# Performance work log

Measured on AMD Instinct MI355X. Metric: run time of the kernel, lower is better.

## Reference

```python
import jax, jax.numpy as jnp
import numpy as np

N, D, GN, UVW = 64, 32, 128, 64
EMB = H = 256
NONSP, SPA = 8, 2
ACT = NONSP + 4          # 12
GOA = 256 + ACT          # fc3 + action = 268
GLO = H + GOA            # 524
SW = 64


def _conv3(x, w, b):
    # 3x3, stride 1, pad 1, NCHW / OIHW (torch layout)
    y = jax.lax.conv_general_dilated(x, w, (1, 1), ((1, 1), (1, 1)),
                                     dimension_numbers=('NCHW', 'OIHW', 'NCHW'))
    return y + b[None, :, None, None]


def _up2(x):
    # bilinear x2, half-pixel centers (matches torch align_corners=False)
    n, c, h, w = x.shape
    return jax.image.resize(x, (n, c, 2 * h, 2 * w), 'bilinear')


def setup_inputs() -> dict:
    key = jax.random.key(0)
    ks = jax.random.split(key, 24)
    def rn(k, shape, s=0.05):
        return jax.random.normal(k, shape, jnp.float32) * s
    G = (jax.random.uniform(ks[0], (N, D, GN, GN)) < 0.1).astype(jnp.float32)
    avail = jax.random.randint(ks[2], (N, NONSP), 0, 2).astype(jnp.int32)
    avail = avail.at[:, 0].set(1)  # guarantee at least one available action
    return {
        'G': G,
        'X': rn(ks[1], (N, D, GN, UVW), 1.0),
        'avail_actions': avail,
        'LSTM_hidden': jnp.zeros((2, 1, N, H), jnp.float32),
        'prev_actions': rn(ks[3], (N, D, ACT), 1.0),
        'relevant_frames': jax.random.randint(ks[4], (N, D), 0, 2).astype(jnp.int32),
        'We': rn(ks[5], (UVW, EMB)), 'be': jnp.zeros((EMB,)),
        'W1': rn(ks[6], (EMB, 256)), 'b1': jnp.zeros((256,)),
        'W2': rn(ks[7], (256, 256)), 'b2': jnp.zeros((256,)),
        'W3': rn(ks[8], (256, 256)), 'b3': jnp.zeros((256,)),
        'Wle': rn(ks[9], (GOA, H)), 'ble': jnp.zeros((H,)),
        'Wih': rn(ks[10], (4 * H, H)), 'Whh': rn(ks[11], (4 * H, H)),
        'bih': jnp.zeros((4 * H,)), 'bhh': jnp.zeros((4 * H,)),
        'Wa': rn(ks[12], (GLO, NONSP)), 'ba': jnp.zeros((NONSP,)),
        'Wv': rn(ks[13], (GLO, 1)), 'bv': jnp.zeros((1,)),
        'Wt1': rn(ks[14], (GLO, 256, 4, 4)), 'bt1': jnp.zeros((256,)),
        'Wc2': rn(ks[15], (128, 256, 3, 3)), 'bc2': jnp.zeros((128,)),
        'Wc3': rn(ks[16], (64, 128, 3, 3)), 'bc3': jnp.zeros((64,)),
        'Wc4': rn(ks[17], (64, 64, 3, 3)), 'bc4': jnp.zeros((64,)),
        'Wc5': rn(ks[18], (64, 64, 3, 3)), 'bc5': jnp.zeros((64,)),
        'Wc6': rn(ks[19], (SPA, 64, 3, 3)), 'bc6': jnp.zeros((SPA,)),
    }


def reference(G, X, avail_actions, LSTM_hidden, prev_actions, relevant_frames,
              We, be, W1, b1, W2, b2, W3, b3, Wle, ble, Wih, Whh, bih, bhh,
              Wa, ba, Wv, bv, Wt1, bt1, Wc2, bc2, Wc3, bc3, Wc4, bc4,
              Wc5, bc5, Wc6, bc6):
    n = G.shape[0]
    eye = jnp.eye(GN, dtype=G.dtype)

    def step(carry, xs):
        h, c, _, _ = carry
        Gc, Xc, pa, rel = xs            # [n,GN,GN], [n,GN,UVW], [n,ACT], [n]
        A = Gc + eye
        dis = 1.0 / jnp.sqrt(jnp.maximum(A.sum(-1), 1.0))
        A_agg = A * dis[:, :, None] * dis[:, None, :]  # D^-1/2 A D^-1/2
        emb = jnp.tanh(Xc @ We + be)
        h1 = jnp.tanh(A_agg @ (emb @ W1 + b1))
        h2 = jnp.tanh(A_agg @ (h1 @ W2 + b2))
        h3 = jnp.tanh(A_agg @ (h2 @ W3 + b3))
        goa = jnp.concatenate([h3.max(axis=1), pa], axis=1)  # [n, GOA]
        xin = jnp.tanh(goa @ Wle + ble)
        gates = xin @ Wih.T + bih + h @ Whh.T + bhh
        i, f, g, o = jnp.split(gates, 4, axis=1)
        c_new = jax.nn.sigmoid(f) * c + jax.nn.sigmoid(i) * jnp.tanh(g)
        h_new = jax.nn.sigmoid(o) * jnp.tanh(c_new)
        keep = (rel != 0).astype(h_new.dtype)[:, None]  # reset hidden for irrelevant frames
        return (h_new * keep, c_new * keep, h_new, goa), None

    h0, c0 = LSTM_hidden[0, 0], LSTM_hidden[1, 0]
    goa0 = jnp.zeros((n, GOA), G.dtype)
    xs = (jnp.swapaxes(G, 0, 1), jnp.swapaxes(X, 0, 1),
          jnp.swapaxes(prev_actions, 0, 1), jnp.swapaxes(relevant_frames, 0, 1))
    (hf, cf, hout, goa), _ = jax.lax.scan(step, (h0, c0, h0, goa0), xs)

    glo = jnp.concatenate([hout, goa], axis=1)  # [n, 524]
    logits = glo @ Wa + ba
    logits = jnp.where(avail_actions == 0, -jnp.inf, logits)
    nonspatial_policy = jax.nn.softmax(logits, axis=1)
    value = glo @ Wv + bv

    # deconv on 1x1 input == einsum with torch [in,out,kh,kw] weight
    s1 = jax.nn.leaky_relu(jnp.einsum('nc,cfhw->nfhw', glo, Wt1) + bt1[None, :, None, None], 0.1)
    # note: original F.relu(x, 0.1) is plain relu (0.1 lands in `inplace`)
    s2 = jax.nn.relu(_up2(_conv3(s1, Wc2, bc2)))
    s3 = jax.nn.relu(_up2(_conv3(s2, Wc3, bc3)))
    s4 = jax.nn.relu(_up2(_conv3(s3, Wc4, bc4)))
    s5 = jax.nn.relu(_up2(_conv3(s4, Wc5, bc5)))
    sl = _conv3(s5, Wc6, bc6).reshape(n, SPA, -1)
    spatial_policy = jax.nn.softmax(sl, axis=2).reshape(n, SPA, SW, SW)

    LSTM_hidden_out = jnp.stack([hf, cf])[:, None]  # [2,1,n,H]
    return (spatial_policy, nonspatial_policy, value, LSTM_hidden_out)
```

## Files before the change

### kernel.cpp

```cpp
#include <hip/hip_runtime.h>
#include <math.h>

typedef unsigned short u16;
typedef unsigned int u32;

typedef __attribute__((ext_vector_type(8))) short bf16x8;
typedef __attribute__((ext_vector_type(4))) float f32x4;

__device__ __forceinline__ float b2f(u16 u) {
    union { u32 ui; float f; } v; v.ui = ((u32)u) << 16; return v.f;
}
__device__ __forceinline__ float b2f_lo(u32 u) {
    union { u32 ui; float f; } v; v.ui = u << 16; return v.f;
}
__device__ __forceinline__ float b2f_hi(u32 u) {
    union { u32 ui; float f; } v; v.ui = u & 0xffff0000u; return v.f;
}
__device__ __forceinline__ u16 f2b(float f) {
    union { float f; u32 ui; } v; v.f = f;
    u32 x = v.ui;
    u32 r = (x + 0x7fffu + ((x >> 16) & 1u)) >> 16;
    return (u16)r;
}
__device__ __forceinline__ float sigf(float x) { return 1.0f / (1.0f + expf(-x)); }
__device__ __forceinline__ float ftanh(float x) {
    float e = __expf(2.0f * x);
    return 1.0f - 2.0f / (e + 1.0f);
}

#define GNODES 128
#define EMBD   256
#define NB     64
#define TS     32
#define GOA    268
#define GLO    524

#define OUT_SPATIAL 0
#define OUT_NS      524288
#define OUT_V       524800
#define OUT_H       524864

#define WS_GOA   ((size_t)0)
#define WS_HBUF  ((size_t)2195456)
#define WS_CBUF  ((size_t)2260992)
#define WS_HOUT  ((size_t)2326528)
#define WS_GLO   ((size_t)2392064)
#define WS_WIHT  ((size_t)2526208)
#define WS_WHHT  ((size_t)3574784)
#define WS_BSUM  ((size_t)4623360)
#define WS_C2    ((size_t)4627456)
#define WS_C3    ((size_t)4889600)
#define WS_C4    ((size_t)5413888)
#define WS_C5    ((size_t)7511040)
#define WS_SL    ((size_t)15899648)
#define WS_WET   ((size_t)16948224)
#define WS_W1T   ((size_t)16980992)
#define WS_W2T   ((size_t)17112064)
#define WS_W3T   ((size_t)17243136)
#define WS_GX    ((size_t)17374208)
#define WS_S1F   ((size_t)25762816)

#define WS_WP4   WS_GOA
#define WS_WP5   (WS_GOA + (size_t)196608)
#define WS_WP3   (WS_GOA + (size_t)393216)
#define WS_WP2   WS_GX

#define SA_S 264
#define TT_S 136
#define XS_S 72

__global__ void wprep(const float* __restrict__ We, const float* __restrict__ W1,
                      const float* __restrict__ W2, const float* __restrict__ W3,
                      u16* __restrict__ WeT, u16* __restrict__ W1T,
                      u16* __restrict__ W2T, u16* __restrict__ W3T)
{
    int idx = blockIdx.x * 256 + threadIdx.x;
    if (idx < 16384) {
        int k = idx >> 8, nn = idx & 255;
        WeT[nn * 64 + k] = f2b(We[idx]);
    }
    {
        int k = idx >> 8, nn = idx & 255;
        W1T[nn * 256 + k] = f2b(W1[idx]);
        W2T[nn * 256 + k] = f2b(W2[idx]);
        W3T[nn * 256 + k] = f2b(W3[idx]);
    }
}

__global__ __launch_bounds__(1024, 4) void gcn_mfma(
    const float* __restrict__ G, const float* __restrict__ X, const float* __restrict__ pa,
    const u16* __restrict__ WeT, const float* __restrict__ be,
    const u16* __restrict__ W1T, const float* __restrict__ b1,
    const u16* __restrict__ W2T, const float* __restrict__ b2,
    const u16* __restrict__ W3T, const float* __restrict__ b3,
    float* __restrict__ goaAll)
{
    __shared__ u16 Sa[128 * SA_S];
    __shared__ u16 Tt[256 * TT_S];
    __shared__ float dis[GNODES];
    __shared__ float dred[1024];
    __shared__ float pm[256];

    const int item = blockIdx.x;
    const int tid  = threadIdx.x;
    const int wv   = tid >> 6;
    const int nt   = wv & 7;
    const int ch   = wv >> 3;
    const int lane = tid & 63;
    const int l16  = lane & 15;
    const int quad = lane >> 4;
    const float* Gp = G + (size_t)item * GNODES * GNODES;
    const float* Xp = X + (size_t)item * GNODES * 64;

    for (int idx = tid; idx < 128 * 64; idx += 1024) {
        int m = idx >> 6, k = idx & 63;
        Tt[m * XS_S + k] = f2b(Xp[idx]);
    }
    {
        int row = tid >> 3, part = tid & 7;
        const float4* gr = (const float4*)(Gp + (size_t)row * GNODES) + part * 4;
        float s = 0.f;
#pragma unroll
        for (int k = 0; k < 4; ++k) { float4 g = gr[k]; s += g.x + g.y + g.z + g.w; }
        dred[tid] = s;
    }
    __syncthreads();
    if (tid < GNODES) {
        float s = 0.f;
#pragma unroll
        for (int p = 0; p < 8; ++p) s += dred[tid * 8 + p];
        dis[tid] = 1.0f / sqrtf(s + 1.0f);
    }
    __syncthreads();

    bf16x8 bAgg[4];
    {
        const int i = nt * 16 + l16;
        const float di = dis[i];
        const float* gr = Gp + (size_t)i * GNODES;
#pragma unroll
        for (int t = 0; t < 4; ++t) {
            const int k0 = t * 32 + quad * 8;
            float4 ga = *(const float4*)(gr + k0);
            float4 gb = *(const float4*)(gr + k0 + 4);
            float vv[8] = {ga.x, ga.y, ga.z, ga.w, gb.x, gb.y, gb.z, gb.w};
            bf16x8 f;
#pragma unroll
            for (int j = 0; j < 8; ++j) {
                int k = k0 + j;
                float a = (vv[j] + (k == i ? 1.0f : 0.0f)) * di * dis[k];
                f[j] = (short)f2b(a);
            }
            bAgg[t] = f;
        }
    }

    {
        bf16x8 a0 = *(const bf16x8*)(Tt + (16 * nt + l16) * XS_S + quad * 8);
        bf16x8 a1 = *(const bf16x8*)(Tt + (16 * nt + l16) * XS_S + 32 + quad * 8);
        for (int cj = 0; cj < 8; ++cj) {
            const int ct = ch * 8 + cj;
            const int nf = ct * 16 + l16;
            bf16x8 wb0 = *(const bf16x8*)(WeT + nf * 64 + quad * 8);
            bf16x8 wb1 = *(const bf16x8*)(WeT + nf * 64 + 32 + quad * 8);
            float bb = be[nf];
            f32x4 acc = {bb, bb, bb, bb};
            acc = __builtin_amdgcn_mfma_f32_16x16x32_bf16(a0, wb0, acc, 0, 0, 0);
            acc = __builtin_amdgcn_mfma_f32_16x16x32_bf16(a1, wb1, acc, 0, 0, 0);
#pragma unroll
            for (int r = 0; r < 4; ++r) {
                int node = 16 * nt + quad * 4 + r;
                Sa[node * SA_S + nf] = f2b(ftanh(acc[r]));
            }
        }
    }
    __syncthreads();

    const u16* WTs[3]  = {W1T, W2T, W3T};
    const float* bss[3] = {b1, b2, b3};

    for (int l = 0; l < 3; ++l) {
        const u16* WT = WTs[l];
        const float* bias = bss[l];

        const int nf = wv * 16 + l16;
        const float bb = bias[nf];
        bf16x8 bfr[8];
#pragma unroll
        for (int t = 0; t < 8; ++t)
            bfr[t] = *(const bf16x8*)(WT + (size_t)nf * 256 + t * 32 + quad * 8);

        for (int rt = 0; rt < 8; ++rt) {
            bf16x8 afr[8];
#pragma unroll
            for (int t = 0; t < 8; ++t)
                afr[t] = *(const bf16x8*)(Sa + (16 * rt + l16) * SA_S + t * 32 + quad * 8);
            f32x4 acc = {bb, bb, bb, bb};
#pragma unroll
            for (int t = 0; t < 8; ++t)
                acc = __builtin_amdgcn_mfma_f32_16x16x32_bf16(afr[t], bfr[t], acc, 0, 0, 0);
            u16 p0 = f2b(acc[0]), p1 = f2b(acc[1]), p2 = f2b(acc[2]), p3 = f2b(acc[3]);
            uint2 pk; pk.x = (u32)p0 | ((u32)p1 << 16); pk.y = (u32)p2 | ((u32)p3 << 16);
            *(uint2*)(Tt + (size_t)nf * TT_S + 16 * rt + quad * 4) = pk;
        }
        __syncthreads();

        for (int fj = 0; fj < 8; ++fj) {
            const int ft = ch * 8 + fj;
            bf16x8 afr[4];
#pragma unroll
            for (int t = 0; t < 4; ++t)
                afr[t] = *(const bf16x8*)(Tt + (16 * ft + l16) * TT_S + t * 32 + quad * 8);
            f32x4 acc = {0.f, 0.f, 0.f, 0.f};
#pragma unroll
            for (int t = 0; t < 4; ++t)
                acc = __builtin_amdgcn_mfma_f32_16x16x32_bf16(afr[t], bAgg[t], acc, 0, 0, 0);
            int i = nt * 16 + l16;
            u16 p0 = f2b(ftanh(acc[0])), p1 = f2b(ftanh(acc[1]));
            u16 p2 = f2b(ftanh(acc[2])), p3 = f2b(ftanh(acc[3]));
            uint2 pk; pk.x = (u32)p0 | ((u32)p1 << 16); pk.y = (u32)p2 | ((u32)p3 << 16);
            *(uint2*)(Sa + (size_t)i * SA_S + 16 * ft + quad * 4) = pk;
        }
        __syncthreads();
    }

    const int nb = item >> 5, tt = item & 31;
    float* gdst = goaAll + ((size_t)tt * NB + nb) * GOA;
    float mymax = -2.0f;
    if (tid < 512) {
        int f = tid & 255, h = tid >> 8;
        for (int i = h * 64; i < h * 64 + 64; ++i)
            mymax = fmaxf(mymax, b2f(Sa[i * SA_S + f]));
        if (h == 1) pm[f] = mymax;
    }
    __syncthreads();
    if (tid < 256) {
        gdst[tid] = fmaxf(mymax, pm[tid]);
    } else if (tid >= 512 && tid < 524) {
        gdst[256 + (tid - 512)] = pa[(size_t)item * 12 + (tid - 512)];
    }
}

__global__ void wtrans(const float* __restrict__ Wih, const float* __restrict__ Whh,
                       const float* __restrict__ bih, const float* __restrict__ bhh,
                       float* __restrict__ wihT, float* __restrict__ whh4, float* __restrict__ bsum)
{
    int idx = blockIdx.x * 256 + threadIdx.x;
    int r = idx >> 8;
    int k = idx & 255;
    wihT[k * 1024 + r] = Wih[idx];
    whh4[(size_t)(k >> 2) * 4096 + r * 4 + (k & 3)] = Whh[idx];
    if (idx < 1024) bsum[idx] = bih[idx] + bhh[idx];
}

#define LP_IT 4
__global__ __launch_bounds__(256) void lstm_pre(
    const float* __restrict__ goaAll, const float* __restrict__ Wle, const float* __restrict__ ble,
    const float* __restrict__ wihT, const float* __restrict__ bsum,
    float* __restrict__ gatesX)
{
    __shared__ float glT[GOA * LP_IT];
    __shared__ float xvT[256 * LP_IT];
    const int b0 = blockIdx.x * LP_IT;
    const int u = threadIdx.x;

    for (int idx = u; idx < LP_IT * GOA; idx += 256) {
        int k = idx >> 2, it = idx & 3;
        glT[idx] = goaAll[(size_t)(b0 + it) * GOA + k];
    }
    __syncthreads();

    {
        float acc[LP_IT];
        float bl = ble[u];
#pragma unroll
        for (int i = 0; i < LP_IT; ++i) acc[i] = bl;
        for (int k = 0; k < GOA; ++k) {
            float w = Wle[k * 256 + u];
            float4 g4 = *(const float4*)&glT[k * 4];
            acc[0] = fmaf(g4.x, w, acc[0]);
            acc[1] = fmaf(g4.y, w, acc[1]);
            acc[2] = fmaf(g4.z, w, acc[2]);
            acc[3] = fmaf(g4.w, w, acc[3]);
        }
        float4 xv4;
        xv4.x = tanhf(acc[0]); xv4.y = tanhf(acc[1]);
        xv4.z = tanhf(acc[2]); xv4.w = tanhf(acc[3]);
        *(float4*)&xvT[u * 4] = xv4;
    }
    __syncthreads();

    {
        float a[4][LP_IT];
#pragma unroll
        for (int g = 0; g < 4; ++g) {
            float bs = bsum[g * 256 + u];
#pragma unroll
            for (int i = 0; i < LP_IT; ++i) a[g][i] = bs;
        }
        for (int k = 0; k < 256; ++k) {
            float4 x4 = *(const float4*)&xvT[k * 4];
            float w0 = wihT[k * 1024 + u];
            float w1 = wihT[k * 1024 + 256 + u];
            float w2 = wihT[k * 1024 + 512 + u];
            float w3 = wihT[k * 1024 + 768 + u];
            a[0][0] = fmaf(x4.x, w0, a[0][0]); a[0][1] = fmaf(x4.y, w0, a[0][1]);
            a[0][2] = fmaf(x4.z, w0, a[0][2]); a[0][3] = fmaf(x4.w, w0, a[0][3]);
            a[1][0] = fmaf(x4.x, w1, a[1][0]); a[1][1] = fmaf(x4.y, w1, a[1][1]);
            a[1][2] = fmaf(x4.z, w1, a[1][2]); a[1][3] = fmaf(x4.w, w1, a[1][3]);
            a[2][0] = fmaf(x4.x, w2, a[2][0]); a[2][1] = fmaf(x4.y, w2, a[2][1]);
            a[2][2] = fmaf(x4.z, w2, a[2][2]); a[2][3] = fmaf(x4.w, w2, a[2][3]);
            a[3][0] = fmaf(x4.x, w3, a[3][0]); a[3][1] = fmaf(x4.y, w3, a[3][1]);
            a[3][2] = fmaf(x4.z, w3, a[3][2]); a[3][3] = fmaf(x4.w, w3, a[3][3]);
        }
#pragma unroll
        for (int g = 0; g < 4; ++g)
#pragma unroll
            for (int i = 0; i < LP_IT; ++i)
                gatesX[(size_t)(b0 + i) * 1024 + g * 256 + u] = a[g][i];
    }
}

__global__ __launch_bounds__(1024) void lstm_seq(
    const float* __restrict__ gatesX, const float* __restrict__ whh4,
    const int* __restrict__ relf, const float* __restrict__ lh,
    float* __restrict__ hbuf, float* __restrict__ cbuf, float* __restrict__ hout)
{
    __shared__ float hv[256];
    __shared__ float ga[1024];
    __shared__ int hzf;
    const int n = blockIdx.x, u = threadIdx.x;
    float cpriv = 0.f;
    if (u < 256) { hv[u] = lh[n * 256 + u]; cpriv = lh[16384 + n * 256 + u]; }
    if (u == 0) hzf = 0;
    __syncthreads();

    const float4* w4base = (const float4*)whh4 + u;

    for (int t = 0; t < TS; ++t) {
        float a = gatesX[((size_t)t * NB + n) * 1024 + u];
        if (!hzf) {
            float a0 = 0.f, a1 = 0.f, a2 = 0.f, a3 = 0.f;
#pragma unroll 4
            for (int k4 = 0; k4 < 64; ++k4) {
                float4 w = w4base[k4 * 1024];
                int k = k4 * 4;
                a0 = fmaf(hv[k],     w.x, a0);
                a1 = fmaf(hv[k + 1], w.y, a1);
                a2 = fmaf(hv[k + 2], w.z, a2);
                a3 = fmaf(hv[k + 3], w.w, a3);
            }
            a += (a0 + a1) + (a2 + a3);
        }
        ga[u] = a;
        __syncthreads();
        if (u < 256) {
            float ai = ga[u], af = ga[256 + u], ag = ga[512 + u], ao = ga[768 + u];
            float cn = sigf(af) * cpriv + sigf(ai) * tanhf(ag);
            float hn = sigf(ao) * tanhf(cn);
            float kp = (relf[n * TS + t] != 0) ? 1.f : 0.f;
            if (t == TS - 1) {
                hout[n * 256 + u] = hn;
                hbuf[n * 256 + u] = hn * kp;
                cbuf[n * 256 + u] = cn * kp;
            }
            cpriv = cn * kp;
            hv[u] = hn * kp;
        }
        if (u == 0) hzf = (relf[n * TS + t] != 0) ? 0 : 1;
        __syncthreads();
    }
}

__global__ __launch_bounds__(256) void heads(
    const float* __restrict__ goaAll, const float* __restrict__ hout,
    const float* __restrict__ hbuf, const float* __restrict__ cbuf,
    const float* __restrict__ Wa, const float* __restrict__ ba,
    const float* __restrict__ Wv, const float* __restrict__ bv,
    const int* __restrict__ avail, float* __restrict__ glo, float* __restrict__ out)
{
    __shared__ float gl[GLO];
    __shared__ float lg[8];
    const int n = blockIdx.x, tid = threadIdx.x;
    const float* gsrc = goaAll + ((size_t)31 * NB + n) * GOA;
    gl[tid] = hout[n * 256 + tid];
    gl[256 + tid] = gsrc[tid];
    if (tid < 12) gl[512 + tid] = gsrc[256 + tid];
    __syncthreads();

    glo[n * GLO + tid]       = gl[tid];
    glo[n * GLO + 256 + tid] = gl[256 + tid];
    if (tid < 12) glo[n * GLO + 512 + tid] = gl[512 + tid];

    out[OUT_H + n * 256 + tid]         = hbuf[n * 256 + tid];
    out[OUT_H + 16384 + n * 256 + tid] = cbuf[n * 256 + tid];

    if (tid < 8) {
        float a = ba[tid];
        for (int k = 0; k < GLO; ++k) a = fmaf(gl[k], Wa[k * 8 + tid], a);
        lg[tid] = (avail[n * 8 + tid] == 0) ? -INFINITY : a;
    } else if (tid == 8) {
        float a = bv[0];
        for (int k = 0; k < GLO; ++k) a = fmaf(gl[k], Wv[k], a);
        out[OUT_V + n] = a;
    }
    __syncthreads();
    if (tid == 0) {
        float m = -INFINITY;
        for (int a = 0; a < 8; ++a) m = fmaxf(m, lg[a]);
        float e[8], s = 0.f;
        for (int a = 0; a < 8; ++a) { e[a] = expf(lg[a] - m); s += e[a]; }
        float inv = 1.f / s;
        for (int a = 0; a < 8; ++a) out[OUT_NS + n * 8 + a] = e[a] * inv;
    }
}

__global__ void wpad_k(const float* __restrict__ Wc4, const float* __restrict__ Wc5,
                       const float* __restrict__ Wc3, const float* __restrict__ Wc2,
                       float* __restrict__ wp4, float* __restrict__ wp5,
                       float* __restrict__ wp3, float* __restrict__ wp2)
{
    int idx = blockIdx.x * 256 + threadIdx.x;
    const float* src; float* dst; int r;
    if (idx < 36864)        { src = Wc4; dst = wp4; r = idx; }
    else if (idx < 73728)   { src = Wc5; dst = wp5; r = idx - 36864; }
    else if (idx < 147456)  { src = Wc3; dst = wp3; r = idx - 73728; }
    else                    { src = Wc2; dst = wp2; r = idx - 147456; }
    int pair = r / 9, q = r - pair * 9;
    dst[pair * 12 + q] = src[r];
}

__global__ __launch_bounds__(512) void deconv1_k(
    const float* __restrict__ glo, const float* __restrict__ Wt1, const float* __restrict__ bt1,
    float* __restrict__ s1f)
{
    const int f = blockIdx.x;
    const int tid = threadIdx.x;
    const int n = tid >> 3, pp = tid & 7;
    float bb = bt1[f];
    float a0 = bb, a1 = bb;
    const float* gp = glo + n * GLO;
    for (int c = 0; c < GLO; ++c) {
        float g = gp[c];
        float2 w2 = *(const float2*)&Wt1[(((size_t)c * 256 + f) << 4) + pp * 2];
        a0 = fmaf(g, w2.x, a0);
        a1 = fmaf(g, w2.y, a1);
    }
    float* dst = s1f + (((size_t)n * 256 + f) << 4) + pp * 2;
    dst[0] = a0 > 0.f ? a0 : 0.1f * a0;
    dst[1] = a1 > 0.f ? a1 : 0.1f * a1;
}

__global__ __launch_bounds__(256) void conv2_k(
    const float* __restrict__ s1f, const float* __restrict__ wp2, const float* __restrict__ bc2,
    u16* __restrict__ c2)
{
    __shared__ float sp[256 * 36];
    const int n = blockIdx.x >> 3, cot = blockIdx.x & 7;
    const int tid = threadIdx.x;
    for (int i = tid; i < 256 * 36; i += 256) sp[i] = 0.f;
    __syncthreads();
    for (int i = tid; i < 4096; i += 256) {
        int ci = i >> 4, p = i & 15, y = p >> 2, x = p & 3;
        sp[ci * 36 + (y + 1) * 6 + (x + 1)] = s1f[((size_t)n * 256 + ci) * 16 + p];
    }
    __syncthreads();

    const int co = cot * 16 + (tid >> 4);
    const int p = tid & 15, y = p >> 2, x = p & 3;
    float acc = bc2[co];
    const float* wpb = wp2 + (size_t)co * 256 * 12;
    for (int ci = 0; ci < 256; ++ci) {
        const float4* wv4 = (const float4*)(wpb + ci * 12);
        float4 w0 = wv4[0], w1 = wv4[1], w2 = wv4[2];
        float wc[9] = {w0.x, w0.y, w0.z, w0.w, w1.x, w1.y, w1.z, w1.w, w2.x};
        const float* s = sp + ci * 36 + y * 6 + x;
#pragma unroll
        for (int ky = 0; ky < 3; ++ky) {
#pragma unroll
            for (int kx = 0; kx < 3; ++kx)
                acc = fmaf(s[ky * 6 + kx], wc[ky * 3 + kx], acc);
        }
    }
    c2[((size_t)n * 128 + co) * 16 + p] = f2b(acc);
}

template<int CIN, int HI, int WI, int BH, int DW, int COT, int CO>
__global__ __launch_bounds__(256) void up_conv_b(
    const u16* __restrict__ in, const float* __restrict__ wpad, const float* __restrict__ bias,
    u16* __restrict__ out)
{
    constexpr int H2 = 2 * HI, W2 = 2 * WI;
    constexpr int XG = W2 / DW;
    constexpr int ROWS = BH + 2;
    constexpr int STR = W2 + 2;
    constexpr int NBAND = H2 / BH;
    constexpr int CT = CO / COT;
    constexpr int PAIRS = COT / 2;
    static_assert(XG * BH * PAIRS == 256, "thread map must cover block");
    static_assert((STR & 1) == 0, "u32 LDS reads need even u16 stride");

    __shared__ u16 S[CIN * ROWS * STR];

    const int tid = threadIdx.x;
    int b = blockIdx.x;
    const int ct = b % CT; b /= CT;
    const int band = b % NBAND;
    const int n = b / NBAND;
    const int r0 = band * BH;

    const u16* ip = in + (size_t)n * CIN * HI * WI;

    for (int i = tid; i < CIN * ROWS * STR; i += 256) {
        int x  = i % STR;
        int ry = (i / STR) % ROWS;
        int ci = i / (STR * ROWS);
        int yy = r0 - 1 + ry;
        int xx = x - 1;
        float v = 0.f;
        if (yy >= 0 && yy < H2 && xx >= 0 && xx < W2) {
            int y0 = (yy - 1) >> 1; float fy = (yy & 1) ? 0.25f : 0.75f;
            int x0 = (xx - 1) >> 1; float fx = (xx & 1) ? 0.25f : 0.75f;
            int y0c = y0 < 0 ? 0 : y0, y1c = y0 + 1 > HI - 1 ? HI - 1 : y0 + 1;
            int x0c = x0 < 0 ? 0 : x0, x1c = x0 + 1 > WI - 1 ? WI - 1 : x0 + 1;
            const u16* bp = ip + ci * HI * WI;
            float v00 = b2f(bp[y0c * WI + x0c]), v01 = b2f(bp[y0c * WI + x1c]);
            float v10 = b2f(bp[y1c * WI + x0c]), v11 = b2f(bp[y1c * WI + x1c]);
            v = (1.f - fy) * ((1.f - fx) * v00 + fx * v01)
              +        fy  * ((1.f - fx) * v10 + fx * v11);
            v = fmaxf(v, 0.f);
        }
        S[i] = f2b(v);
    }
    __syncthreads();

    const int xg = tid % XG;
    const int y  = (tid / XG) % BH;
    const int pr = tid / (XG * BH);
    const int co0 = ct * COT + pr * 2;
    const int x0 = xg * DW;
    const int yo = r0 + y;

    float acc0[DW], acc1[DW];
    const float bb0 = bias[co0], bb1 = bias[co0 + 1];
#pragma unroll
    for (int d = 0; d < DW; ++d) { acc0[d] = bb0; acc1[d] = bb1; }

    const float* wp0 = wpad + (size_t)(co0 * CIN) * 12;
    const float* wp1 = wpad + (size_t)((co0 + 1) * CIN) * 12;

    for (int ci = 0; ci < CIN; ++ci) {
        float wa[9], wb[9];
        {
            const float4* av = (const float4*)(wp0 + ci * 12);
            float4 a0 = av[0], a1 = av[1], a2 = av[2];
            wa[0] = a0.x; wa[1] = a0.y; wa[2] = a0.z; wa[3] = a0.w;
            wa[4] = a1.x; wa[5] = a1.y; wa[6] = a1.z; wa[7] = a1.w; wa[8] = a2.x;
            const float4* bv = (const float4*)(wp1 + ci * 12);
            float4 b0 = bv[0], b1 = bv[1], b2v = bv[2];
            wb[0] = b0.x; wb[1] = b0.y; wb[2] = b0.z; wb[3] = b0.w;
            wb[4] = b1.x; wb[5] = b1.y; wb[6] = b1.z; wb[7] = b1.w; wb[8] = b2v.x;
        }
#pragma unroll
        for (int ky = 0; ky < 3; ++ky) {
            const u32* Sr = (const u32*)(S + ci * ROWS * STR + (y + ky) * STR + x0);
            float seg[DW + 2];
#pragma unroll
            for (int k = 0; k < (DW + 2) / 2; ++k) {
                u32 u = Sr[k];
                seg[2 * k]     = b2f_lo(u);
                seg[2 * k + 1] = b2f_hi(u);
            }
#pragma unroll
            for (int d = 0; d < DW; ++d) {
                acc0[d] = fmaf(seg[d],     wa[ky * 3 + 0], acc0[d]);
                acc0[d] = fmaf(seg[d + 1], wa[ky * 3 + 1], acc0[d]);
                acc0[d] = fmaf(seg[d + 2], wa[ky * 3 + 2], acc0[d]);
                acc1[d] = fmaf(seg[d],     wb[ky * 3 + 0], acc1[d]);
                acc1[d] = fmaf(seg[d + 1], wb[ky * 3 + 1], acc1[d]);
                acc1[d] = fmaf(seg[d + 2], wb[ky * 3 + 2], acc1[d]);
            }
        }
    }

    u16* op0 = out + (((size_t)(n * CO + co0) * H2) + yo) * W2 + x0;
    u16* op1 = op0 + (size_t)H2 * W2;
#pragma unroll
    for (int d = 0; d < DW; d += 2) {
        u32 p0 = (u32)f2b(acc0[d]) | ((u32)f2b(acc0[d + 1]) << 16);
        u32 p1 = (u32)f2b(acc1[d]) | ((u32)f2b(acc1[d + 1]) << 16);
        *(u32*)(op0 + d) = p0;
        *(u32*)(op1 + d) = p1;
    }
}

__global__ __launch_bounds__(256) void up_conv6(
    const u16* __restrict__ c5, const float* __restrict__ w, const float* __restrict__ bias,
    u16* __restrict__ sl)
{
    __shared__ u16 S[40960];
    const int tid = threadIdx.x;
    const int n = blockIdx.x >> 3;
    const int band = blockIdx.x & 7;
    const int r0 = band * 8;
    const u16* ip = c5 + (size_t)n * 64 * 1024;

    for (int i = tid; i < 40960; i += 256) {
        int x2 = i & 63; int ry = (i >> 6) % 10; int ci = i / 640;
        int yy = r0 - 1 + ry;
        float v = 0.f;
        if (yy >= 0 && yy < 64) {
            int y0 = (yy - 1) >> 1; float fy = (yy & 1) ? 0.25f : 0.75f;
            int x0 = (x2 - 1) >> 1; float fx = (x2 & 1) ? 0.25f : 0.75f;
            int y0c = y0 < 0 ? 0 : y0, y1c = y0 + 1 > 31 ? 31 : y0 + 1;
            int x0c = x0 < 0 ? 0 : x0, x1c = x0 + 1 > 31 ? 31 : x0 + 1;
            const u16* b = ip + ci * 1024;
            float v00 = b2f(b[y0c * 32 + x0c]), v01 = b2f(b[y0c * 32 + x1c]);
            float v10 = b2f(b[y1c * 32 + x0c]), v11 = b2f(b[y1c * 32 + x1c]);
            v = fmaxf((1.f - fy) * ((1.f - fx) * v00 + fx * v01)
                      +      fy  * ((1.f - fx) * v10 + fx * v11), 0.f);
        }
        S[i] = f2b(v);
    }
    __syncthreads();

    {
        const int u = tid;
        const int x0p = (u & 15) * 4;
        const int yr  = (u >> 4) & 7;
        const int co  = u >> 7;
        const int y = r0 + yr;
        float acc[4];
        float bb = bias[co];
#pragma unroll
        for (int d = 0; d < 4; ++d) acc[d] = bb;
        const float* wp = w + (size_t)co * 64 * 9;
        for (int ci = 0; ci < 64; ++ci) {
            const u16* Sr = S + ci * 640;
            float wk[9];
#pragma unroll
            for (int q = 0; q < 9; ++q) wk[q] = wp[ci * 9 + q];
#pragma unroll
            for (int ky = 0; ky < 3; ++ky) {
                int ry = yr + ky;
                float seg[6];
#pragma unroll
                for (int dx = 0; dx < 6; ++dx) {
                    int xx = x0p + dx - 1;
                    seg[dx] = (xx >= 0 && xx < 64) ? b2f(Sr[ry * 64 + xx]) : 0.f;
                }
#pragma unroll
                for (int d = 0; d < 4; ++d) {
                    acc[d] = fmaf(seg[d],     wk[ky * 3 + 0], acc[d]);
                    acc[d] = fmaf(seg[d + 1], wk[ky * 3 + 1], acc[d]);
                    acc[d] = fmaf(seg[d + 2], wk[ky * 3 + 2], acc[d]);
                }
            }
        }
        u16* op = sl + (size_t)(n * 2 + co) * 4096 + y * 64 + x0p;
        u32 p0 = (u32)f2b(acc[0]) | ((u32)f2b(acc[1]) << 16);
        u32 p1 = (u32)f2b(acc[2]) | ((u32)f2b(acc[3]) << 16);
        *(u32*)(op)     = p0;
        *(u32*)(op + 2) = p1;
    }
}

__global__ __launch_bounds__(256) void softmax_spatial(const u16* __restrict__ sl, float* __restrict__ out)
{
    __shared__ float red[256];
    const int b = blockIdx.x;
    const u16* src = sl + (size_t)b * 4096;
    float* dst = out + (size_t)b * 4096;
    const int tid = threadIdx.x;
    float m = -INFINITY;
    for (int i = tid; i < 4096; i += 256) m = fmaxf(m, b2f(src[i]));
    red[tid] = m; __syncthreads();
    for (int s = 128; s > 0; s >>= 1) { if (tid < s) red[tid] = fmaxf(red[tid], red[tid + s]); __syncthreads(); }
    m = red[0]; __syncthreads();
    float sum = 0.f;
    for (int i = tid; i < 4096; i += 256) sum += expf(b2f(src[i]) - m);
    red[tid] = sum; __syncthreads();
    for (int s = 128; s > 0; s >>= 1) { if (tid < s) red[tid] += red[tid + s]; __syncthreads(); }
    float inv = 1.f / red[0];
    for (int i = tid; i < 4096; i += 256) dst[i] = expf(b2f(src[i]) - m) * inv;
}

extern "C" void kernel_launch(void* const* d_in, const int* in_sizes, int n_in,
                              void* d_out, int out_size, void* d_ws, size_t ws_size,
                              hipStream_t stream)
{
    const float* G     = (const float*)d_in[0];
    const float* X     = (const float*)d_in[1];
    const int*   avail = (const int*)d_in[2];
    const float* lh    = (const float*)d_in[3];
    const float* pa    = (const float*)d_in[4];
    const int*   relf  = (const int*)d_in[5];
    const float* We  = (const float*)d_in[6];   const float* be  = (const float*)d_in[7];
    const float* W1  = (const float*)d_in[8];   const float* b1  = (const float*)d_in[9];
    const float* W2  = (const float*)d_in[10];  const float* b2  = (const float*)d_in[11];
    const float* W3  = (const float*)d_in[12];  const float* b3  = (const float*)d_in[13];
    const float* Wle = (const float*)d_in[14];  const float* ble = (const float*)d_in[15];
    const float* Wih = (const float*)d_in[16];  const float* Whh = (const float*)d_in[17];
    const float* bih = (const float*)d_in[18];  const float* bhh = (const float*)d_in[19];
    const float* Wa  = (const float*)d_in[20];  const float* ba  = (const float*)d_in[21];
    const float* Wv  = (const float*)d_in[22];  const float* bv  = (const float*)d_in[23];
    const float* Wt1 = (const float*)d_in[24];  const float* bt1 = (const float*)d_in[25];
    const float* Wc2 = (const float*)d_in[26];  const float* bc2 = (const float*)d_in[27];
    const float* Wc3 = (const float*)d_in[28];  const float* bc3 = (const float*)d_in[29];
    const float* Wc4 = (const float*)d_in[30];  const float* bc4 = (const float*)d_in[31];
    const float* Wc5 = (const float*)d_in[32];  const float* bc5 = (const float*)d_in[33];
    const float* Wc6 = (const float*)d_in[34];  const float* bc6 = (const float*)d_in[35];

    char* ws = (char*)d_ws;
    float* goaAll = (float*)(ws + WS_GOA);
    float* hbuf   = (float*)(ws + WS_HBUF);
    float* cbuf   = (float*)(ws + WS_CBUF);
    float* hout   = (float*)(ws + WS_HOUT);
    float* glo    = (float*)(ws + WS_GLO);
    float* wihT   = (float*)(ws + WS_WIHT);
    float* whh4   = (float*)(ws + WS_WHHT);
    float* bsum   = (float*)(ws + WS_BSUM);
    u16*   c2     = (u16*)(ws + WS_C2);
    u16*   c3     = (u16*)(ws + WS_C3);
    u16*   c4     = (u16*)(ws + WS_C4);
    u16*   c5     = (u16*)(ws + WS_C5);
    u16*   sl     = (u16*)(ws + WS_SL);
    u16*   WeT    = (u16*)(ws + WS_WET);
    u16*   W1T    = (u16*)(ws + WS_W1T);
    u16*   W2T    = (u16*)(ws + WS_W2T);
    u16*   W3T    = (u16*)(ws + WS_W3T);
    float* gatesX = (float*)(ws + WS_GX);
    float* s1f    = (float*)(ws + WS_S1F);
    float* wp4    = (float*)(ws + WS_WP4);
    float* wp5    = (float*)(ws + WS_WP5);
    float* wp3    = (float*)(ws + WS_WP3);
    float* wp2    = (float*)(ws + WS_WP2);
    float* out    = (float*)d_out;

    wprep<<<256, 256, 0, stream>>>(We, W1, W2, W3, WeT, W1T, W2T, W3T);
    wtrans<<<1024, 256, 0, stream>>>(Wih, Whh, bih, bhh, wihT, whh4, bsum);
    gcn_mfma<<<2048, 1024, 0, stream>>>(G, X, pa, WeT, be, W1T, b1, W2T, b2, W3T, b3, goaAll);
    lstm_pre<<<512, 256, 0, stream>>>(goaAll, Wle, ble, wihT, bsum, gatesX);
    lstm_seq<<<64, 1024, 0, stream>>>(gatesX, whh4, relf, lh, hbuf, cbuf, hout);
    heads<<<64, 256, 0, stream>>>(goaAll, hout, hbuf, cbuf, Wa, ba, Wv, bv, avail, glo, out);
    wpad_k<<<1728, 256, 0, stream>>>(Wc4, Wc5, Wc3, Wc2, wp4, wp5, wp3, wp2);
    deconv1_k<<<256, 512, 0, stream>>>(glo, Wt1, bt1, s1f);
    conv2_k<<<512, 256, 0, stream>>>(s1f, wp2, bc2, c2);
    up_conv_b<128, 4, 4, 8, 4, 32, 64><<<128, 256, 0, stream>>>(c2, wp3, bc3, c3);
    up_conv_b<64, 8, 8, 4, 4, 32, 64><<<512, 256, 0, stream>>>(c3, wp4, bc4, c4);
    up_conv_b<64, 16, 16, 4, 8, 32, 64><<<1024, 256, 0, stream>>>(c4, wp5, bc5, c5);
    up_conv6<<<512, 256, 0, stream>>>(c5, Wc6, bc6, sl);
    softmax_spatial<<<128, 256, 0, stream>>>(sl, out + OUT_SPATIAL);
}
```

Before: 1.313 ms.

## Use bf16 MFMA for the conv4 and conv5 upsample-conv stages

Replaces the scalar FP32 fused upsample+3x3 conv kernels for layers 4 and 5 with an MFMA kernel. Each block stages a bilinear-upsampled, ReLU'd bf16 tile of the input band in swizzled shared memory. The 3x3 conv then runs as nine 16x16x32 bf16 matrix-multiply taps, with the weights pre-transposed to bf16 by a new prep kernel. This aims to cut the FP32 FMA cost of these two conv layers, at the price of bf16 weight rounding and a different shared-memory tiling.

```diff
diff --git a/kernel.cpp b/kernel.cpp
--- a/kernel.cpp
+++ b/kernel.cpp
@@ -415,19 +415,28 @@
     }
 }
 
-__global__ void wpad_k(const float* __restrict__ Wc4, const float* __restrict__ Wc5,
-                       const float* __restrict__ Wc3, const float* __restrict__ Wc2,
-                       float* __restrict__ wp4, float* __restrict__ wp5,
+__global__ void wpad_k(const float* __restrict__ Wc3, const float* __restrict__ Wc2,
                        float* __restrict__ wp3, float* __restrict__ wp2)
 {
     int idx = blockIdx.x * 256 + threadIdx.x;
     const float* src; float* dst; int r;
-    if (idx < 36864)        { src = Wc4; dst = wp4; r = idx; }
-    else if (idx < 73728)   { src = Wc5; dst = wp5; r = idx - 36864; }
-    else if (idx < 147456)  { src = Wc3; dst = wp3; r = idx - 73728; }
-    else                    { src = Wc2; dst = wp2; r = idx - 147456; }
+    if (idx < 73728) { src = Wc3; dst = wp3; r = idx; }
+    else             { src = Wc2; dst = wp2; r = idx - 73728; }
     int pair = r / 9, q = r - pair * 9;
     dst[pair * 12 + q] = src[r];
+}
+
+__global__ void wconvb_k(const float* __restrict__ Wc4, const float* __restrict__ Wc5,
+                         u16* __restrict__ wb4, u16* __restrict__ wb5)
+{
+    int idx = blockIdx.x * 256 + threadIdx.x;
+    int which = idx / 36864;
+    int r = idx - which * 36864;
+    int co = r / 576, rem = r - co * 576;
+    int ci = rem / 9, q = rem - ci * 9;
+    const float* src = which ? Wc5 : Wc4;
+    u16* dst = which ? wb5 : wb4;
+    dst[(q * 64 + co) * 64 + ci] = f2b(src[r]);
 }
 
 __global__ __launch_bounds__(512) void deconv1_k(
@@ -591,6 +600,93 @@
         u32 p1 = (u32)f2b(acc1[d]) | ((u32)f2b(acc1[d + 1]) << 16);
         *(u32*)(op0 + d) = p0;
         *(u32*)(op1 + d) = p1;
+    }
+}
+
+template<int HI>
+__global__ __launch_bounds__(256) void up_conv_mfma(
+    const u16* __restrict__ in, const u16* __restrict__ wq,
+    const float* __restrict__ bias, u16* __restrict__ out)
+{
+    constexpr int H2 = 2 * HI, W2 = 2 * HI;
+    constexpr int BH = 4;
+    constexpr int ROWS = BH + 2;
+    constexpr int STRP = W2 + 2;
+    constexpr int NBAND = H2 / BH;
+    constexpr int XH = W2 / 16;
+    constexpr int NPX = ROWS * STRP;
+
+    __shared__ alignas(16) u16 S[NPX * 64];
+
+    const int tid  = threadIdx.x;
+    const int lane = tid & 63;
+    const int wv   = tid >> 6;
+    const int l16  = lane & 15;
+    const int quad = lane >> 4;
+    const int band = blockIdx.x % NBAND;
+    const int n    = blockIdx.x / NBAND;
+    const int r0   = band * BH;
+    const u16* ip  = in + (size_t)n * 64 * HI * HI;
+
+    for (int i = tid; i < NPX * 64; i += 256) {
+        int ci = i / NPX;
+        int pxl = i - ci * NPX;
+        int ry = pxl / STRP, sx = pxl - ry * STRP;
+        int yy = r0 - 1 + ry, xx = sx - 1;
+        float v = 0.f;
+        if (yy >= 0 && yy < H2 && xx >= 0 && xx < W2) {
+            int y0 = (yy - 1) >> 1; float fy = (yy & 1) ? 0.25f : 0.75f;
+            int x0 = (xx - 1) >> 1; float fx = (xx & 1) ? 0.25f : 0.75f;
+            int y0c = y0 < 0 ? 0 : y0, y1c = y0 + 1 > HI - 1 ? HI - 1 : y0 + 1;
+            int x0c = x0 < 0 ? 0 : x0, x1c = x0 + 1 > HI - 1 ? HI - 1 : x0 + 1;
+            const u16* bp = ip + ci * HI * HI;
+            float v00 = b2f(bp[y0c * HI + x0c]), v01 = b2f(bp[y0c * HI + x1c]);
+            float v10 = b2f(bp[y1c * HI + x0c]), v11 = b2f(bp[y1c * HI + x1c]);
+            v = (1.f - fy) * ((1.f - fx) * v00 + fx * v01)
+              +        fy  * ((1.f - fx) * v10 + fx * v11);
+            v = fmaxf(v, 0.f);
+        }
+        u32 byt = (((u32)pxl << 7) + ((u32)ci << 1)) ^ (((u32)(pxl & 7)) << 4);
+        *(u16*)((char*)S + byt) = f2b(v);
+    }
+    __syncthreads();
+
+    bf16x8 af[9][2];
+#pragma unroll
+    for (int q = 0; q < 9; ++q)
+#pragma unroll
+        for (int kh = 0; kh < 2; ++kh)
+            af[q][kh] = *(const bf16x8*)(wq + ((q * 64 + wv * 16 + l16) * 64 + kh * 32 + quad * 8));
+
+    float b4[4];
+#pragma unroll
+    for (int r = 0; r < 4; ++r) b4[r] = bias[wv * 16 + quad * 4 + r];
+
+    for (int y = 0; y < BH; ++y) {
+        for (int xh = 0; xh < XH; ++xh) {
+            f32x4 acc = {0.f, 0.f, 0.f, 0.f};
+#pragma unroll
+            for (int qy = 0; qy < 3; ++qy) {
+#pragma unroll
+                for (int qx = 0; qx < 3; ++qx) {
+                    const int q = qy * 3 + qx;
+                    const int P = (y + qy) * STRP + xh * 16 + qx + l16;
+                    const u32 base = ((u32)P << 7) + ((u32)quad << 4);
+                    const u32 swz  = ((u32)(P & 7)) << 4;
+                    const bf16x8 bf0 = *(const bf16x8*)((char*)S + (base ^ swz));
+                    const bf16x8 bf1 = *(const bf16x8*)((char*)S + ((base + 64) ^ swz));
+                    acc = __builtin_amdgcn_mfma_f32_16x16x32_bf16(af[q][0], bf0, acc, 0, 0, 0);
+                    acc = __builtin_amdgcn_mfma_f32_16x16x32_bf16(af[q][1], bf1, acc, 0, 0, 0);
+                }
+            }
+            const int xo = xh * 16 + l16;
+            const int yo = r0 + y;
+#pragma unroll
+            for (int r = 0; r < 4; ++r) {
+                const int co = wv * 16 + quad * 4 + r;
+                out[((size_t)(n * 64 + co) * H2 + yo) * W2 + xo] = f2b(acc[r] + b4[r]);
+            }
+        }
     }
 }
 
@@ -731,8 +827,8 @@
     u16*   W3T    = (u16*)(ws + WS_W3T);
     float* gatesX = (float*)(ws + WS_GX);
     float* s1f    = (float*)(ws + WS_S1F);
-    float* wp4    = (float*)(ws + WS_WP4);
-    float* wp5    = (float*)(ws + WS_WP5);
+    u16*   wb4    = (u16*)(ws + WS_WP4);
+    u16*   wb5    = (u16*)(ws + WS_WP5);
     float* wp3    = (float*)(ws + WS_WP3);
     float* wp2    = (float*)(ws + WS_WP2);
     float* out    = (float*)d_out;
@@ -743,12 +839,13 @@
     lstm_pre<<<512, 256, 0, stream>>>(goaAll, Wle, ble, wihT, bsum, gatesX);
     lstm_seq<<<64, 1024, 0, stream>>>(gatesX, whh4, relf, lh, hbuf, cbuf, hout);
     heads<<<64, 256, 0, stream>>>(goaAll, hout, hbuf, cbuf, Wa, ba, Wv, bv, avail, glo, out);
-    wpad_k<<<1728, 256, 0, stream>>>(Wc4, Wc5, Wc3, Wc2, wp4, wp5, wp3, wp2);
+    wpad_k<<<1440, 256, 0, stream>>>(Wc3, Wc2, wp3, wp2);
+    wconvb_k<<<288, 256, 0, stream>>>(Wc4, Wc5, wb4, wb5);
     deconv1_k<<<256, 512, 0, stream>>>(glo, Wt1, bt1, s1f);
     conv2_k<<<512, 256, 0, stream>>>(s1f, wp2, bc2, c2);
     up_conv_b<128, 4, 4, 8, 4, 32, 64><<<128, 256, 0, stream>>>(c2, wp3, bc3, c3);
-    up_conv_b<64, 8, 8, 4, 4, 32, 64><<<512, 256, 0, stream>>>(c3, wp4, bc4, c4);
-    up_conv_b<64, 16, 16, 4, 8, 32, 64><<<1024, 256, 0, stream>>>(c4, wp5, bc5, c5);
+    up_conv_mfma<8><<<256, 256, 0, stream>>>(c3, wb4, bc4, c4);
+    up_conv_mfma<16><<<512, 256, 0, stream>>>(c4, wb5, bc5, c5);
     up_conv6<<<512, 256, 0, stream>>>(c5, Wc6, bc6, sl);
     softmax_spatial<<<128, 256, 0, stream>>>(sl, out + OUT_SPATIAL);
 }
```

Measured after the change: 1.244 ms. -5.2%, faster.
